# Kernel tuning notes

Hardware: AMD Instinct MI355X
Metric: run time of the kernel (lower is better)

The kernel has to match this reference:

```python
import jax, jax.numpy as jnp
import numpy as np

NUM_EMBEDDINGS = 1024
EMBEDDING_DIM = 64

def setup_inputs() -> dict:
    key = jax.random.key(0)
    k1, k2 = jax.random.split(key)
    inputs = jax.random.normal(k1, (32, 64, 64, EMBEDDING_DIM), dtype=jnp.float32)
    # torch init: uniform_(-1/K, 1/K)
    embedding = jax.random.uniform(
        k2, (NUM_EMBEDDINGS, EMBEDDING_DIM), dtype=jnp.float32,
        minval=-1.0 / NUM_EMBEDDINGS, maxval=1.0 / NUM_EMBEDDINGS)
    return {"inputs": inputs, "embedding": embedding}

def reference(inputs, embedding):
    input_shape = inputs.shape
    d = embedding.shape[1]
    K = embedding.shape[0]
    flat = inputs.reshape(-1, d)                                  # [N, d]
    distances = (jnp.sum(flat ** 2, axis=1, keepdims=True)
                 + jnp.sum(embedding ** 2, axis=1)
                 - 2.0 * jnp.matmul(flat, embedding.T))
    encoding_indices = jnp.argmin(distances, axis=1)              # [N]
    encodings = jax.nn.one_hot(encoding_indices, K, dtype=inputs.dtype)  # [N, K]
    quantized = jnp.matmul(encodings, embedding).reshape(input_shape)
    quantized_original = quantized
    # straight-through estimator
    quantized_st = inputs + jax.lax.stop_gradient(quantized - inputs)
    avg_probs = jnp.mean(encodings, axis=0)                       # [K]
    perplexity = jnp.exp(-jnp.sum(avg_probs * jnp.log(avg_probs + 1e-10)))
    return (quantized_st, quantized_original, perplexity, encodings)
```

## Files before the change

### kernel.cpp

```cpp
#include <hip/hip_runtime.h>
#include <math.h>

#define N_ROWS   131072
#define D        64
#define K_EMB    1024
#define M_TILE   128
#define KC       128
#define LDSTR    68
#define MARGIN_ACC 1e-6f

#define Q_ST_OFF   0
#define Q_OR_OFF   8388608
#define PERP_OFF   16777216
#define ENC_OFF    16777217


__global__ __launch_bounds__(256) void enorm32_kernel(const float* __restrict__ emb,
                                                      float* __restrict__ enorm) {
    int k = blockIdx.x * 256 + threadIdx.x;
    const float4* row = reinterpret_cast<const float4*>(emb + (size_t)k * D);
    float s = 0.f;
#pragma unroll
    for (int i = 0; i < 16; ++i) {
        float4 v = row[i];
        s = fmaf(v.x, v.x, s); s = fmaf(v.y, v.y, s);
        s = fmaf(v.z, v.z, s); s = fmaf(v.w, v.w, s);
    }
    enorm[k] = s;
}

__global__ __launch_bounds__(256) void vq_main(const float* __restrict__ in,
                                               const float* __restrict__ emb,
                                               const float* __restrict__ enorm32,
                                               unsigned int* __restrict__ counts,
                                               unsigned int* __restrict__ flagcount,
                                               int* __restrict__ flaglist,
                                               int flagcap,
                                               float* __restrict__ out) {
    __shared__ __align__(16) float Xs[M_TILE][LDSTR];
    __shared__ __align__(16) float Es[KC][LDSTR];
    __shared__ __align__(16) float enorms[K_EMB];
    __shared__ int bks[M_TILE];

    const int tid  = threadIdx.x;
    const int tc   = tid & 15;
    const int trf  = tid >> 4;
    const int base = blockIdx.x * M_TILE;

    {
        float4 v = *reinterpret_cast<const float4*>(enorm32 + tid * 4);
        *reinterpret_cast<float4*>(&enorms[tid * 4]) = v;
    }
    {
        const float4* src = reinterpret_cast<const float4*>(in + (size_t)base * D);
#pragma unroll
        for (int i = 0; i < 8; ++i) {
            int lin = i * 256 + tid;
            float4 v = src[lin];
            *reinterpret_cast<float4*>(&Xs[lin >> 4][(lin & 15) << 2]) = v;
        }
    }

    float b1[8], b2[8]; int k1[8];
#pragma unroll
    for (int j = 0; j < 8; ++j) { b1[j] = -1e30f; b2[j] = -1e30f; k1[j] = 0; }

    const float* xsb = &Xs[trf][0];
    const float* esb = &Es[tc][0];

    for (int ch = 0; ch < K_EMB / KC; ++ch) {
        __syncthreads();
        {
            const float4* esrc = reinterpret_cast<const float4*>(emb + (size_t)ch * KC * D);
#pragma unroll
            for (int i = 0; i < 8; ++i) {
                int lin = i * 256 + tid;
                float4 v = esrc[lin];
                *reinterpret_cast<float4*>(&Es[lin >> 4][(lin & 15) << 2]) = v;
            }
        }
        __syncthreads();

        float acc[8][8];
#pragma unroll
        for (int c = 0; c < 8; ++c) {
            float nh = -0.5f * enorms[ch * KC + tc + 16 * c];
#pragma unroll
            for (int j = 0; j < 8; ++j) acc[j][c] = nh;
        }

#pragma unroll 1
        for (int db = 0; db < 16; ++db) {
            float4 e4[8];
#pragma unroll
            for (int c = 0; c < 8; ++c)
                e4[c] = *reinterpret_cast<const float4*>(esb + c * (16 * LDSTR) + db * 4);
#pragma unroll
            for (int j = 0; j < 8; ++j) {
                float4 x4 = *reinterpret_cast<const float4*>(xsb + j * (16 * LDSTR) + db * 4);
#pragma unroll
                for (int c = 0; c < 8; ++c) {
                    acc[j][c] = fmaf(x4.x, e4[c].x, acc[j][c]);
                    acc[j][c] = fmaf(x4.y, e4[c].y, acc[j][c]);
                    acc[j][c] = fmaf(x4.z, e4[c].z, acc[j][c]);
                    acc[j][c] = fmaf(x4.w, e4[c].w, acc[j][c]);
                }
            }
            asm volatile("" ::: "memory");
        }

#pragma unroll
        for (int c = 0; c < 8; ++c) {
            int k = ch * KC + tc + 16 * c;
#pragma unroll
            for (int j = 0; j < 8; ++j) {
                float s = acc[j][c];
                if (s > b1[j]) { b2[j] = b1[j]; b1[j] = s; k1[j] = k; }
                else if (s > b2[j]) b2[j] = s;
            }
        }
    }

#pragma unroll
    for (int j = 0; j < 8; ++j) {
        float v = b1[j], v2 = b2[j]; int kk = k1[j];
#pragma unroll
        for (int off = 8; off >= 1; off >>= 1) {
            float ov  = __shfl_xor(v,  off, 64);
            int   ok  = __shfl_xor(kk, off, 64);
            float ov2 = __shfl_xor(v2, off, 64);
            bool win = (ov > v) || (ov == v && ok < kk);
            float loser = win ? v : ov;
            v2 = fmaxf(fmaxf(v2, ov2), loser);
            if (win) { v = ov; kk = ok; }
        }
        if (tc == 0) {
            int row = trf + 16 * j;
            bks[row] = kk;
            if (v - v2 < MARGIN_ACC) {
                int pos = (int)atomicAdd(flagcount, 1u);
                if (pos < flagcap) flaglist[pos] = ((base + row) << 10) | kk;
            }
        }
    }

    {
        float* ep = out + ENC_OFF + (size_t)base * K_EMB;
        float4 z = make_float4(0.f, 0.f, 0.f, 0.f);
        float4* ap = reinterpret_cast<float4*>(ep + 3);
        for (int i = tid; i < 32767; i += 256) ap[i] = z;
        if (tid == 0) { ep[0] = 0.f; ep[1] = 0.f; ep[2] = 0.f; ep[131071] = 0.f; }
    }
    __syncthreads();

    if (tid < M_TILE) {
        int kk = bks[tid];
        atomicAdd(&counts[kk], 1u);
        out[ENC_OFF + (size_t)(base + tid) * K_EMB + kk] = 1.0f;
    }
    {
        int row = tid >> 1;
        int p   = tid & 1;
        int kk  = bks[row];
        const float4* er = reinterpret_cast<const float4*>(emb + (size_t)kk * D);
        float4* o1 = reinterpret_cast<float4*>(out + Q_ST_OFF + (size_t)(base + row) * D);
        float4* o2 = reinterpret_cast<float4*>(out + Q_OR_OFF + (size_t)(base + row) * D);
#pragma unroll
        for (int i = 0; i < 8; ++i) {
            float4 v = er[p * 8 + i];
            o1[p * 8 + i] = v;
            o2[p * 8 + i] = v;
        }
    }
}

__global__ __launch_bounds__(256) void rescore_kernel(const float* __restrict__ in,
                                                      const float* __restrict__ emb,
                                                      const unsigned int* __restrict__ flagcount,
                                                      const int* __restrict__ flaglist,
                                                      int flagcap,
                                                      unsigned int* __restrict__ counts,
                                                      float* __restrict__ out) {
    __shared__ __align__(16) float xs[64];
    __shared__ double rv[4];
    __shared__ int    rk[4];
    __shared__ int    oldk_s;

    const int tid = threadIdx.x;
    int nf = (int)*flagcount;
    bool overflow = nf > flagcap;
    int total = overflow ? N_ROWS : nf;

    for (int idx = blockIdx.x; idx < total; idx += gridDim.x) {
        int row, oldk;
        if (!overflow) {
            int e = flaglist[idx];
            row = e >> 10; oldk = e & 1023;
        } else {
            row = idx; oldk = -1;
        }
        if (tid < 16)
            *reinterpret_cast<float4*>(&xs[tid * 4]) =
                reinterpret_cast<const float4*>(in + (size_t)row * D)[tid];
        __syncthreads();
        if (overflow) {
            const float* er = out + ENC_OFF + (size_t)row * K_EMB;
#pragma unroll
            for (int c = 0; c < 4; ++c)
                if (er[tid * 4 + c] == 1.0f) oldk_s = tid * 4 + c;
            __syncthreads();
            oldk = oldk_s;
        }

        double bv = 1e300; int bk = 0;
#pragma unroll
        for (int c = 0; c < 4; ++c) {
            int k = tid * 4 + c;
            const float4* er = reinterpret_cast<const float4*>(emb + (size_t)k * D);
            double dot = 0.0, en = 0.0;
#pragma unroll 4
            for (int i = 0; i < 16; ++i) {
                float4 ev = er[i];
                float4 xv = *reinterpret_cast<const float4*>(&xs[i * 4]);
                double e0 = ev.x, e1 = ev.y, e2 = ev.z, e3 = ev.w;
                en  = fma(e0, e0, en);  en  = fma(e1, e1, en);
                en  = fma(e2, e2, en);  en  = fma(e3, e3, en);
                dot = fma((double)xv.x, e0, dot); dot = fma((double)xv.y, e1, dot);
                dot = fma((double)xv.z, e2, dot); dot = fma((double)xv.w, e3, dot);
            }
            double s = fma(-2.0, dot, en);
            if (s < bv) { bv = s; bk = k; }
        }
        const int lane = tid & 63, wv = tid >> 6;
        {
            double v = bv; int kk = bk;
#pragma unroll
            for (int off = 32; off >= 1; off >>= 1) {
                double ov = __shfl_xor(v, off, 64);
                int    ok = __shfl_xor(kk, off, 64);
                if (ov < v || (ov == v && ok < kk)) { v = ov; kk = ok; }
            }
            if (lane == 0) { rv[wv] = v; rk[wv] = kk; }
        }
        __syncthreads();
        if (tid == 0) {
            double v = rv[0]; int kk = rk[0];
#pragma unroll
            for (int w = 1; w < 4; ++w) {
                double ov = rv[w]; int ok = rk[w];
                if (ov < v || (ov == v && ok < kk)) { v = ov; kk = ok; }
            }
            if (kk != oldk) {
                out[ENC_OFF + (size_t)row * K_EMB + oldk] = 0.0f;
                out[ENC_OFF + (size_t)row * K_EMB + kk]   = 1.0f;
                atomicAdd(&counts[oldk], (unsigned int)-1);
                atomicAdd(&counts[kk], 1u);
                const float4* er = reinterpret_cast<const float4*>(emb + (size_t)kk * D);
                float4* o1 = reinterpret_cast<float4*>(out + Q_ST_OFF + (size_t)row * D);
                float4* o2 = reinterpret_cast<float4*>(out + Q_OR_OFF + (size_t)row * D);
#pragma unroll
                for (int i = 0; i < 16; ++i) { float4 vv = er[i]; o1[i] = vv; o2[i] = vv; }
            }
        }
        __syncthreads();
    }
}

__global__ __launch_bounds__(1024) void perp_kernel(const unsigned int* __restrict__ counts,
                                                    float* __restrict__ out_perp) {
    const int k = threadIdx.x;
    double p = (double)counts[k] * (1.0 / (double)N_ROWS);
    double t = p * log(p + 1e-10);
#pragma unroll
    for (int off = 32; off >= 1; off >>= 1) t += __shfl_down(t, off, 64);
    __shared__ double red[16];
    if ((k & 63) == 0) red[k >> 6] = t;
    __syncthreads();
    if (k < 16) {
        double s = red[k];
#pragma unroll
        for (int off = 8; off >= 1; off >>= 1) s += __shfl_down(s, off, 16);
        if (k == 0) out_perp[0] = (float)exp(-s);
    }
}

extern "C" void kernel_launch(void* const* d_in, const int* in_sizes, int n_in,
                              void* d_out, int out_size, void* d_ws, size_t ws_size,
                              hipStream_t stream) {
    const float* in  = (const float*)d_in[0];
    const float* emb = (const float*)d_in[1];
    float* out = (float*)d_out;
    unsigned int* counts    = (unsigned int*)d_ws;
    unsigned int* flagcount = (unsigned int*)((char*)d_ws + 4096);
    float* enorm32          = (float*)((char*)d_ws + 8192);
    int*   flaglist         = (int*)((char*)d_ws + 16384);
    int flagcap = (ws_size > 16384) ? (int)((ws_size - 16384) / 4) : 0;
    if (flagcap > N_ROWS) flagcap = N_ROWS;

    hipMemsetAsync(d_ws, 0, 8192, stream);
    enorm32_kernel<<<K_EMB / 256, 256, 0, stream>>>(emb, enorm32);
    vq_main<<<N_ROWS / M_TILE, 256, 0, stream>>>(in, emb, enorm32, counts,
                                                 flagcount, flaglist, flagcap, out);
    rescore_kernel<<<1024, 256, 0, stream>>>(in, emb, flagcount, flaglist, flagcap,
                                             counts, out);
    perp_kernel<<<1, 1024, 0, stream>>>(counts, out + PERP_OFF);
}
```

Before: 902.3 us.

## Compute distances with split-bf16 MFMA and fuse near-tie rescoring into main kernel

Replaces the scalar fp32 FMA distance GEMM with bf16 32x32x16 MFMA instructions. Inputs and codebook are split into hi/lo bf16 parts and three MFMA products are accumulated to approximate fp32 precision. Near-tie rows are now flagged in shared memory and rescored in double precision inside the same block before the outputs are written, which removes the separate rescore kernel and the duplicate writes it made. The cost is per-chunk bf16 conversion work, a wider tie margin that will flag more rows, and serial per-block rescoring that can stall blocks with many ties.

```diff
diff --git a/kernel.cpp b/kernel.cpp
--- a/kernel.cpp
+++ b/kernel.cpp
@@ -1,19 +1,31 @@
 #include <hip/hip_runtime.h>
 #include <math.h>
 
-#define N_ROWS   131072
-#define D        64
-#define K_EMB    1024
-#define M_TILE   128
-#define KC       128
-#define LDSTR    68
-#define MARGIN_ACC 1e-6f
-
-#define Q_ST_OFF   0
-#define Q_OR_OFF   8388608
-#define PERP_OFF   16777216
-#define ENC_OFF    16777217
-
+#define N_ROWS 131072
+#define D      64
+#define K_EMB  1024
+#define M_TILE 128
+#define KC     128
+#define XSTR   72
+#define MARGIN_D 1e-5f
+
+#define Q_ST_OFF 0
+#define Q_OR_OFF 8388608
+#define PERP_OFF 16777216
+#define ENC_OFF  16777217
+
+
+typedef __attribute__((ext_vector_type(8)))  short bf16x8;
+typedef __attribute__((ext_vector_type(16))) float f32x16;
+
+__device__ __forceinline__ unsigned short f2bf_rne(float f) {
+    unsigned int u = __float_as_uint(f);
+    unsigned int r = u + 0x7fffu + ((u >> 16) & 1u);
+    return (unsigned short)(r >> 16);
+}
+__device__ __forceinline__ float bf2f(unsigned short h) {
+    return __uint_as_float(((unsigned int)h) << 16);
+}
 
 __global__ __launch_bounds__(256) void enorm32_kernel(const float* __restrict__ emb,
                                                       float* __restrict__ enorm) {
@@ -33,23 +45,31 @@
                                                const float* __restrict__ emb,
                                                const float* __restrict__ enorm32,
                                                unsigned int* __restrict__ counts,
-                                               unsigned int* __restrict__ flagcount,
-                                               int* __restrict__ flaglist,
-                                               int flagcap,
                                                float* __restrict__ out) {
-    __shared__ __align__(16) float Xs[M_TILE][LDSTR];
-    __shared__ __align__(16) float Es[KC][LDSTR];
-    __shared__ __align__(16) float enorms[K_EMB];
+    __shared__ __align__(16) unsigned short XH[M_TILE * XSTR];
+    __shared__ __align__(16) unsigned short XL[M_TILE * XSTR];
+    __shared__ __align__(16) unsigned short EH[KC * XSTR];
+    __shared__ __align__(16) unsigned short EL[KC * XSTR];
+    __shared__ __align__(16) float en_s[K_EMB];
+    __shared__ __align__(16) float xs2[D];
     __shared__ int bks[M_TILE];
+    __shared__ int flagl[M_TILE];
+    __shared__ int nflag;
+    __shared__ double rv[4];
+    __shared__ int    rk[4];
 
     const int tid  = threadIdx.x;
-    const int tc   = tid & 15;
-    const int trf  = tid >> 4;
+    const int lane = tid & 63;
+    const int w    = tid >> 6;
+    const int hl   = lane >> 5;
+    const int l31  = lane & 31;
     const int base = blockIdx.x * M_TILE;
-
+    const int wrow = w * 32;
+
+    if (tid == 0) nflag = 0;
     {
         float4 v = *reinterpret_cast<const float4*>(enorm32 + tid * 4);
-        *reinterpret_cast<float4*>(&enorms[tid * 4]) = v;
+        *reinterpret_cast<float4*>(&en_s[tid * 4]) = v;
     }
     {
         const float4* src = reinterpret_cast<const float4*>(in + (size_t)base * D);
@@ -57,17 +77,34 @@
         for (int i = 0; i < 8; ++i) {
             int lin = i * 256 + tid;
             float4 v = src[lin];
-            *reinterpret_cast<float4*>(&Xs[lin >> 4][(lin & 15) << 2]) = v;
-        }
-    }
-
-    float b1[8], b2[8]; int k1[8];
-#pragma unroll
-    for (int j = 0; j < 8; ++j) { b1[j] = -1e30f; b2[j] = -1e30f; k1[j] = 0; }
-
-    const float* xsb = &Xs[trf][0];
-    const float* esb = &Es[tc][0];
-
+            int row = lin >> 4, c4 = lin & 15;
+            ushort4 h, l;
+            h.x = f2bf_rne(v.x); l.x = f2bf_rne(v.x - bf2f(h.x));
+            h.y = f2bf_rne(v.y); l.y = f2bf_rne(v.y - bf2f(h.y));
+            h.z = f2bf_rne(v.z); l.z = f2bf_rne(v.z - bf2f(h.z));
+            h.w = f2bf_rne(v.w); l.w = f2bf_rne(v.w - bf2f(h.w));
+            *reinterpret_cast<ushort4*>(&XH[row * XSTR + c4 * 4]) = h;
+            *reinterpret_cast<ushort4*>(&XL[row * XSTR + c4 * 4]) = l;
+        }
+    }
+    __syncthreads();
+
+    bf16x8 AH[4], AL[4];
+    {
+        const unsigned short* xh = &XH[(wrow + l31) * XSTR + hl * 8];
+        const unsigned short* xl = &XL[(wrow + l31) * XSTR + hl * 8];
+#pragma unroll
+        for (int kb = 0; kb < 4; ++kb) {
+            AH[kb] = *reinterpret_cast<const bf16x8*>(xh + kb * 16);
+            AL[kb] = *reinterpret_cast<const bf16x8*>(xl + kb * 16);
+        }
+    }
+
+    float b1[16], b2[16]; int k1[16];
+#pragma unroll
+    for (int r = 0; r < 16; ++r) { b1[r] = 1e30f; b2[r] = 1e30f; k1[r] = 0; }
+
+#pragma unroll 1
     for (int ch = 0; ch < K_EMB / KC; ++ch) {
         __syncthreads();
         {
@@ -76,70 +113,70 @@
             for (int i = 0; i < 8; ++i) {
                 int lin = i * 256 + tid;
                 float4 v = esrc[lin];
-                *reinterpret_cast<float4*>(&Es[lin >> 4][(lin & 15) << 2]) = v;
-            }
-        }
-        __syncthreads();
-
-        float acc[8][8];
-#pragma unroll
-        for (int c = 0; c < 8; ++c) {
-            float nh = -0.5f * enorms[ch * KC + tc + 16 * c];
-#pragma unroll
-            for (int j = 0; j < 8; ++j) acc[j][c] = nh;
-        }
-
-#pragma unroll 1
-        for (int db = 0; db < 16; ++db) {
-            float4 e4[8];
-#pragma unroll
-            for (int c = 0; c < 8; ++c)
-                e4[c] = *reinterpret_cast<const float4*>(esb + c * (16 * LDSTR) + db * 4);
-#pragma unroll
-            for (int j = 0; j < 8; ++j) {
-                float4 x4 = *reinterpret_cast<const float4*>(xsb + j * (16 * LDSTR) + db * 4);
-#pragma unroll
-                for (int c = 0; c < 8; ++c) {
-                    acc[j][c] = fmaf(x4.x, e4[c].x, acc[j][c]);
-                    acc[j][c] = fmaf(x4.y, e4[c].y, acc[j][c]);
-                    acc[j][c] = fmaf(x4.z, e4[c].z, acc[j][c]);
-                    acc[j][c] = fmaf(x4.w, e4[c].w, acc[j][c]);
-                }
+                int row = lin >> 4, c4 = lin & 15;
+                ushort4 h, l;
+                h.x = f2bf_rne(v.x); l.x = f2bf_rne(v.x - bf2f(h.x));
+                h.y = f2bf_rne(v.y); l.y = f2bf_rne(v.y - bf2f(h.y));
+                h.z = f2bf_rne(v.z); l.z = f2bf_rne(v.z - bf2f(h.z));
+                h.w = f2bf_rne(v.w); l.w = f2bf_rne(v.w - bf2f(h.w));
+                *reinterpret_cast<ushort4*>(&EH[row * XSTR + c4 * 4]) = h;
+                *reinterpret_cast<ushort4*>(&EL[row * XSTR + c4 * 4]) = l;
+            }
+        }
+        __syncthreads();
+
+#pragma unroll 1
+        for (int sub = 0; sub < 4; ++sub) {
+            const unsigned short* eh = &EH[(sub * 32 + l31) * XSTR + hl * 8];
+            const unsigned short* el = &EL[(sub * 32 + l31) * XSTR + hl * 8];
+            bf16x8 BH[4], BL[4];
+#pragma unroll
+            for (int kb = 0; kb < 4; ++kb) {
+                BH[kb] = *reinterpret_cast<const bf16x8*>(eh + kb * 16);
+                BL[kb] = *reinterpret_cast<const bf16x8*>(el + kb * 16);
+            }
+            f32x16 acc = {};
+#pragma unroll
+            for (int kb = 0; kb < 4; ++kb)
+                acc = __builtin_amdgcn_mfma_f32_32x32x16_bf16(AH[kb], BH[kb], acc, 0, 0, 0);
+#pragma unroll
+            for (int kb = 0; kb < 4; ++kb)
+                acc = __builtin_amdgcn_mfma_f32_32x32x16_bf16(AH[kb], BL[kb], acc, 0, 0, 0);
+#pragma unroll
+            for (int kb = 0; kb < 4; ++kb)
+                acc = __builtin_amdgcn_mfma_f32_32x32x16_bf16(AL[kb], BH[kb], acc, 0, 0, 0);
+
+            int kg = ch * KC + sub * 32 + l31;
+            float en = en_s[kg];
+#pragma unroll
+            for (int r = 0; r < 16; ++r) {
+                float s = fmaf(-2.f, acc[r], en);
+                if (s < b1[r]) { b2[r] = b1[r]; b1[r] = s; k1[r] = kg; }
+                else if (s < b2[r]) b2[r] = s;
             }
             asm volatile("" ::: "memory");
         }
-
-#pragma unroll
-        for (int c = 0; c < 8; ++c) {
-            int k = ch * KC + tc + 16 * c;
-#pragma unroll
-            for (int j = 0; j < 8; ++j) {
-                float s = acc[j][c];
-                if (s > b1[j]) { b2[j] = b1[j]; b1[j] = s; k1[j] = k; }
-                else if (s > b2[j]) b2[j] = s;
-            }
-        }
-    }
-
-#pragma unroll
-    for (int j = 0; j < 8; ++j) {
-        float v = b1[j], v2 = b2[j]; int kk = k1[j];
-#pragma unroll
-        for (int off = 8; off >= 1; off >>= 1) {
+    }
+
+#pragma unroll
+    for (int r = 0; r < 16; ++r) {
+        float v = b1[r], v2 = b2[r]; int kk = k1[r];
+#pragma unroll
+        for (int off = 16; off >= 1; off >>= 1) {
             float ov  = __shfl_xor(v,  off, 64);
             int   ok  = __shfl_xor(kk, off, 64);
             float ov2 = __shfl_xor(v2, off, 64);
-            bool win = (ov > v) || (ov == v && ok < kk);
+            bool win = (ov < v) || (ov == v && ok < kk);
             float loser = win ? v : ov;
-            v2 = fmaxf(fmaxf(v2, ov2), loser);
+            v2 = fminf(fminf(v2, ov2), loser);
             if (win) { v = ov; kk = ok; }
         }
-        if (tc == 0) {
-            int row = trf + 16 * j;
+        if (l31 == 0) {
+            int row = wrow + (r & 3) + 8 * (r >> 2) + 4 * hl;
             bks[row] = kk;
-            if (v - v2 < MARGIN_ACC) {
-                int pos = (int)atomicAdd(flagcount, 1u);
-                if (pos < flagcap) flaglist[pos] = ((base + row) << 10) | kk;
+            if (v2 - v < MARGIN_D) {
+                int p = atomicAdd(&nflag, 1);
+                flagl[p] = row;
             }
         }
     }
@@ -153,67 +190,16 @@
     }
     __syncthreads();
 
-    if (tid < M_TILE) {
-        int kk = bks[tid];
-        atomicAdd(&counts[kk], 1u);
-        out[ENC_OFF + (size_t)(base + tid) * K_EMB + kk] = 1.0f;
-    }
-    {
-        int row = tid >> 1;
-        int p   = tid & 1;
-        int kk  = bks[row];
-        const float4* er = reinterpret_cast<const float4*>(emb + (size_t)kk * D);
-        float4* o1 = reinterpret_cast<float4*>(out + Q_ST_OFF + (size_t)(base + row) * D);
-        float4* o2 = reinterpret_cast<float4*>(out + Q_OR_OFF + (size_t)(base + row) * D);
-#pragma unroll
-        for (int i = 0; i < 8; ++i) {
-            float4 v = er[p * 8 + i];
-            o1[p * 8 + i] = v;
-            o2[p * 8 + i] = v;
-        }
-    }
-}
-
-__global__ __launch_bounds__(256) void rescore_kernel(const float* __restrict__ in,
-                                                      const float* __restrict__ emb,
-                                                      const unsigned int* __restrict__ flagcount,
-                                                      const int* __restrict__ flaglist,
-                                                      int flagcap,
-                                                      unsigned int* __restrict__ counts,
-                                                      float* __restrict__ out) {
-    __shared__ __align__(16) float xs[64];
-    __shared__ double rv[4];
-    __shared__ int    rk[4];
-    __shared__ int    oldk_s;
-
-    const int tid = threadIdx.x;
-    int nf = (int)*flagcount;
-    bool overflow = nf > flagcap;
-    int total = overflow ? N_ROWS : nf;
-
-    for (int idx = blockIdx.x; idx < total; idx += gridDim.x) {
-        int row, oldk;
-        if (!overflow) {
-            int e = flaglist[idx];
-            row = e >> 10; oldk = e & 1023;
-        } else {
-            row = idx; oldk = -1;
-        }
+    int nf = nflag;
+#pragma unroll 1
+    for (int fi = 0; fi < nf; ++fi) {
+        int row = flagl[fi];
         if (tid < 16)
-            *reinterpret_cast<float4*>(&xs[tid * 4]) =
-                reinterpret_cast<const float4*>(in + (size_t)row * D)[tid];
-        __syncthreads();
-        if (overflow) {
-            const float* er = out + ENC_OFF + (size_t)row * K_EMB;
-#pragma unroll
-            for (int c = 0; c < 4; ++c)
-                if (er[tid * 4 + c] == 1.0f) oldk_s = tid * 4 + c;
-            __syncthreads();
-            oldk = oldk_s;
-        }
-
+            *reinterpret_cast<float4*>(&xs2[tid * 4]) =
+                reinterpret_cast<const float4*>(in + (size_t)(base + row) * D)[tid];
+        __syncthreads();
         double bv = 1e300; int bk = 0;
-#pragma unroll
+#pragma unroll 1
         for (int c = 0; c < 4; ++c) {
             int k = tid * 4 + c;
             const float4* er = reinterpret_cast<const float4*>(emb + (size_t)k * D);
@@ -221,7 +207,7 @@
 #pragma unroll 4
             for (int i = 0; i < 16; ++i) {
                 float4 ev = er[i];
-                float4 xv = *reinterpret_cast<const float4*>(&xs[i * 4]);
+                float4 xv = *reinterpret_cast<const float4*>(&xs2[i * 4]);
                 double e0 = ev.x, e1 = ev.y, e2 = ev.z, e3 = ev.w;
                 en  = fma(e0, e0, en);  en  = fma(e1, e1, en);
                 en  = fma(e2, e2, en);  en  = fma(e3, e3, en);
@@ -231,7 +217,6 @@
             double s = fma(-2.0, dot, en);
             if (s < bv) { bv = s; bk = k; }
         }
-        const int lane = tid & 63, wv = tid >> 6;
         {
             double v = bv; int kk = bk;
 #pragma unroll
@@ -240,29 +225,39 @@
                 int    ok = __shfl_xor(kk, off, 64);
                 if (ov < v || (ov == v && ok < kk)) { v = ov; kk = ok; }
             }
-            if (lane == 0) { rv[wv] = v; rk[wv] = kk; }
+            if (lane == 0) { rv[w] = v; rk[w] = kk; }
         }
         __syncthreads();
         if (tid == 0) {
             double v = rv[0]; int kk = rk[0];
 #pragma unroll
-            for (int w = 1; w < 4; ++w) {
-                double ov = rv[w]; int ok = rk[w];
+            for (int x = 1; x < 4; ++x) {
+                double ov = rv[x]; int ok = rk[x];
                 if (ov < v || (ov == v && ok < kk)) { v = ov; kk = ok; }
             }
-            if (kk != oldk) {
-                out[ENC_OFF + (size_t)row * K_EMB + oldk] = 0.0f;
-                out[ENC_OFF + (size_t)row * K_EMB + kk]   = 1.0f;
-                atomicAdd(&counts[oldk], (unsigned int)-1);
-                atomicAdd(&counts[kk], 1u);
-                const float4* er = reinterpret_cast<const float4*>(emb + (size_t)kk * D);
-                float4* o1 = reinterpret_cast<float4*>(out + Q_ST_OFF + (size_t)row * D);
-                float4* o2 = reinterpret_cast<float4*>(out + Q_OR_OFF + (size_t)row * D);
-#pragma unroll
-                for (int i = 0; i < 16; ++i) { float4 vv = er[i]; o1[i] = vv; o2[i] = vv; }
-            }
-        }
-        __syncthreads();
+            bks[row] = kk;
+        }
+        __syncthreads();
+    }
+
+    if (tid < M_TILE) {
+        int kk = bks[tid];
+        atomicAdd(&counts[kk], 1u);
+        out[ENC_OFF + (size_t)(base + tid) * K_EMB + kk] = 1.0f;
+    }
+    {
+        int row = tid >> 1;
+        int p   = tid & 1;
+        int kk  = bks[row];
+        const float4* er = reinterpret_cast<const float4*>(emb + (size_t)kk * D);
+        float4* o1 = reinterpret_cast<float4*>(out + Q_ST_OFF + (size_t)(base + row) * D);
+        float4* o2 = reinterpret_cast<float4*>(out + Q_OR_OFF + (size_t)(base + row) * D);
+#pragma unroll
+        for (int i = 0; i < 8; ++i) {
+            float4 v = er[p * 8 + i];
+            o1[p * 8 + i] = v;
+            o2[p * 8 + i] = v;
+        }
     }
 }
 
@@ -290,18 +285,11 @@
     const float* in  = (const float*)d_in[0];
     const float* emb = (const float*)d_in[1];
     float* out = (float*)d_out;
-    unsigned int* counts    = (unsigned int*)d_ws;
-    unsigned int* flagcount = (unsigned int*)((char*)d_ws + 4096);
-    float* enorm32          = (float*)((char*)d_ws + 8192);
-    int*   flaglist         = (int*)((char*)d_ws + 16384);
-    int flagcap = (ws_size > 16384) ? (int)((ws_size - 16384) / 4) : 0;
-    if (flagcap > N_ROWS) flagcap = N_ROWS;
-
-    hipMemsetAsync(d_ws, 0, 8192, stream);
+    unsigned int* counts = (unsigned int*)d_ws;
+    float* enorm32       = (float*)((char*)d_ws + 8192);
+
+    hipMemsetAsync(d_ws, 0, 4096, stream);
     enorm32_kernel<<<K_EMB / 256, 256, 0, stream>>>(emb, enorm32);
-    vq_main<<<N_ROWS / M_TILE, 256, 0, stream>>>(in, emb, enorm32, counts,
-                                                 flagcount, flaglist, flagcap, out);
-    rescore_kernel<<<1024, 256, 0, stream>>>(in, emb, flagcount, flaglist, flagcap,
-                                             counts, out);
+    vq_main<<<N_ROWS / M_TILE, 256, 0, stream>>>(in, emb, enorm32, counts, out);
     perp_kernel<<<1, 1024, 0, stream>>>(counts, out + PERP_OFF);
 }
```

After: 840.1 us. -6.9%, faster.
